# Performance work log

Measured on AMD Instinct MI355X. Metric: run time of the kernel, lower is better.

## Reference

```python
import jax, jax.numpy as jnp
import numpy as np

NUM_CODES = 1024
CODE_DIM = 256
COMMIT_W = 0.25
EPS = 1e-5
ENT_LO, ENT_HI = 0.5, 0.9
ENT_W = 0.1
VAR_FLOOR = 0.05
VAR_W = 1e-3
DECORR_W = 1e-3


def setup_inputs() -> dict:
    key = jax.random.key(0)
    k1, k2, k3 = jax.random.split(key, 3)
    inputs = jax.random.normal(k1, (16, 2048, CODE_DIM), dtype=jnp.float32)
    weight = jax.random.normal(k2, (NUM_CODES, CODE_DIM), dtype=jnp.float32) * 0.1
    usage_counts = jax.random.uniform(k3, (NUM_CODES,), dtype=jnp.float32)
    return {"inputs": inputs, "weight": weight, "usage_counts": usage_counts}


def reference(inputs, weight, usage_counts):
    K, D = weight.shape
    flat = inputs.reshape(-1, D)  # [N, D]
    # squared euclidean distances [N, K]
    dist = (flat ** 2).sum(axis=1, keepdims=True) - 2.0 * flat @ weight.T + (weight ** 2).sum(axis=1)
    idx = jnp.argmin(dist, axis=1)  # [N]
    quant = weight[idx].reshape(inputs.shape)

    commitment_loss = COMMIT_W * jnp.mean((jax.lax.stop_gradient(quant) - inputs) ** 2)
    # straight-through estimator
    quant_ste = inputs + jax.lax.stop_gradient(quant - inputs)

    # usage entropy regularizer
    probs = usage_counts + EPS
    probs = probs / jnp.maximum(probs.sum(), EPS * K)
    usage_entropy = -jnp.sum(probs * jnp.log(probs + EPS)) / np.log(float(K)).astype(np.float32)
    gap = jnp.where(usage_entropy < ENT_LO, ENT_LO - usage_entropy,
                    jnp.where(usage_entropy > ENT_HI, usage_entropy - ENT_HI, 0.0))
    entropy_loss = ENT_W * gap ** 2

    # variance floor penalty on codebook
    variance = jnp.var(weight, axis=0)
    variance_loss = VAR_W * jnp.mean(jax.nn.relu(VAR_FLOOR - variance))

    # decorrelation penalty
    wc = weight - weight.mean(axis=0, keepdims=True)
    cov = wc.T @ wc / float(K)  # [D, D]
    off_diag = cov - jnp.diag(jnp.diag(cov))
    decorrelation_loss = DECORR_W * jnp.mean(off_diag ** 2)

    total_loss = commitment_loss + entropy_loss + variance_loss + decorrelation_loss
    indices = idx.reshape(inputs.shape[:-1])
    return (quant_ste, indices, total_loss, commitment_loss, entropy_loss,
            variance_loss, decorrelation_loss, usage_entropy)
```

## Files before the change

### kernel.cpp

```cpp
#include <hip/hip_runtime.h>
#include <math.h>

#define DIMS   256
#define KCODES 1024
#define NTOT   32768
#define TAU    4.0e-4f

typedef __bf16 bf16x8 __attribute__((ext_vector_type(8)));
typedef float  f32x4  __attribute__((ext_vector_type(4)));

#define WS_COMMIT   0
#define WS_FLAGCNT  1
#define WS_DECORR   2
#define WS_COLSUM   16
#define WS_COLSQ    272
#define WS_WSQ      1024
#define WS_XSQ      2048
#define WS_FLAGS    34816
#define WS_CAND1    67584
#define WS_CAND2    329728
#define WS_CANDI    591872
#define WS_WP       854016

#define OUT_Q    0
#define OUT_IDX  8388608
#define OUT_SCAL 8421376


__global__ __launch_bounds__(256) void prep_kernel(const float* __restrict__ X,
                                                   const float* __restrict__ W,
                                                   __bf16* __restrict__ Xp,
                                                   __bf16* __restrict__ Wp2,
                                                   float* ws) {
  int b = blockIdx.x;
  int tid = threadIdx.x;
  if (b < 1056) {
    __shared__ float sqred[256];
    bool isW = b >= 1024;
    const float* src = isW ? W : X;
    __bf16* dst = isW ? Wp2 : Xp;
    int sqoff = isW ? WS_WSQ : WS_XSQ;
    int bb = isW ? b - 1024 : b;
    int kt = tid >> 5, mtl = (tid >> 4) & 1, lc = tid & 15;
    int row = bb * 32 + mtl * 16 + lc;
    int bt = row >> 7, c = row & 127;
    int wv = c >> 6, t = (c >> 4) & 3;
    size_t hibase = ((((size_t)(bt * 8 + kt) * 2 + wv) * 4 + t) * 2) * 512;
    const float* s = src + (size_t)row * DIMS + kt * 32;
    float sq = 0.f;
    #pragma unroll
    for (int kq = 0; kq < 4; kq++) {
      float4 u = *(const float4*)(s + kq * 8);
      float4 v = *(const float4*)(s + kq * 8 + 4);
      float f[8] = {u.x, u.y, u.z, u.w, v.x, v.y, v.z, v.w};
      bf16x8 hi, lo;
      #pragma unroll
      for (int e = 0; e < 8; e++) {
        __bf16 h = (__bf16)f[e];
        hi[e] = h;
        lo[e] = (__bf16)(f[e] - (float)h);
        sq = fmaf(f[e], f[e], sq);
      }
      size_t off = (size_t)(kq * 16 + lc) * 8;
      *(bf16x8*)&dst[hibase + off] = hi;
      *(bf16x8*)&dst[hibase + 512 + off] = lo;
    }
    sqred[tid] = sq;
    __syncthreads();
    if (tid < 32) {
      float s8 = 0.f;
      #pragma unroll
      for (int k = 0; k < 8; k++) s8 += sqred[k * 32 + tid];
      ws[sqoff + bb * 32 + tid] = s8;
    }
  } else {
    __shared__ float wi_s[KCODES];
    __shared__ float red2[256];
    __shared__ float miB;
    __shared__ float red[4];
    int i0 = b - 1056;
    #pragma unroll
    for (int q = 0; q < 4; q++) {
      int row = q * 256 + tid;
      wi_s[row] = W[(size_t)row * DIMS + i0];
    }
    __syncthreads();
    float pm = 0.f;
    #pragma unroll
    for (int q = 0; q < 4; q++) pm += wi_s[tid * 4 + q];
    red2[tid] = pm;
    __syncthreads();
    if (tid == 0) {
      float s = 0.f;
      for (int k = 0; k < 256; k++) s += red2[k];
      miB = s * (1.0f / 1024.0f);
    }
    int j = tid;
    float a0 = 0.f, sj = 0.f, sqj = 0.f;
    for (int k = 0; k < KCODES; k += 4) {
      #pragma unroll
      for (int u = 0; u < 4; u++) {
        float wj = W[(size_t)(k + u) * DIMS + j];
        a0 = fmaf(wi_s[k + u], wj, a0);
        sj += wj;
        sqj = fmaf(wj, wj, sqj);
      }
    }
    if (j == i0) {
      ws[WS_COLSUM + i0] = sj;
      ws[WS_COLSQ + i0] = sqj;
    }
    __syncthreads();
    const float inv = 1.0f / 1024.0f;
    float mj = sj * inv;
    float v = 0.f;
    float c0 = a0 * inv - miB * mj;
    if (i0 != j) v = c0 * c0;
    #pragma unroll
    for (int m = 32; m >= 1; m >>= 1) v += __shfl_xor(v, m);
    if ((j & 63) == 0) red[j >> 6] = v;
    __syncthreads();
    if (j == 0) atomicAdd(&ws[WS_DECORR], (red[0] + red[1]) + (red[2] + red[3]));
  }
}

__global__ __launch_bounds__(256, 2) void pass1_kernel(const __bf16* __restrict__ Xp,
                                                       const __bf16* __restrict__ Wp2,
                                                       float* ws) {
  __shared__ float wsqs[128];
  __shared__ float d1L[256];
  __shared__ float d2L[256];
  __shared__ int   i1L[256];

  int tid = threadIdx.x;
  int lane = tid & 63, wave = tid >> 6;
  int wm = wave >> 1, wn = wave & 1;
  int quad = lane >> 4, col = lane & 15;
  int l = blockIdx.x;
  int x = l & 7;
  int j = l >> 3;
  int bm = x * 32 + (j & 15) + (j >> 7) * 16;
  int bn = (j >> 4) & 7;
  int rowBase = bm * 128, cb = bn * 128;

  if (tid < 128) wsqs[tid] = ws[WS_WSQ + cb + tid];

  f32x4 acc[4][4];
  #pragma unroll
  for (int i = 0; i < 4; i++)
    #pragma unroll
    for (int jj = 0; jj < 4; jj++) acc[i][jj] = (f32x4){0.f, 0.f, 0.f, 0.f};

  const bf16x8* ab = (const bf16x8*)(Xp + (size_t)bm * 65536 + wm * 4096) + lane;
  const bf16x8* bb = (const bf16x8*)(Wp2 + (size_t)bn * 65536 + wn * 4096) + lane;

  bf16x8 Af[2][8], Bf[2][8];
  #pragma unroll
  for (int f = 0; f < 4; f++) {
    Af[0][f * 2] = ab[f * 128];
    Af[0][f * 2 + 1] = ab[f * 128 + 64];
    Bf[0][f * 2] = bb[f * 128];
    Bf[0][f * 2 + 1] = bb[f * 128 + 64];
  }
  #pragma unroll
  for (int kt = 0; kt < 8; kt++) {
    const int cur = kt & 1, nxt = cur ^ 1;
    if (kt < 7) {
      const bf16x8* an = ab + (kt + 1) * 1024;
      const bf16x8* bv = bb + (kt + 1) * 1024;
      #pragma unroll
      for (int f = 0; f < 4; f++) {
        Af[nxt][f * 2] = an[f * 128];
        Af[nxt][f * 2 + 1] = an[f * 128 + 64];
        Bf[nxt][f * 2] = bv[f * 128];
        Bf[nxt][f * 2 + 1] = bv[f * 128 + 64];
      }
    }
    #pragma unroll
    for (int nt = 0; nt < 4; nt++) {
      #pragma unroll
      for (int mt = 0; mt < 4; mt++) {
        acc[mt][nt] = __builtin_amdgcn_mfma_f32_16x16x32_bf16(Af[cur][mt * 2], Bf[cur][nt * 2], acc[mt][nt], 0, 0, 0);
        acc[mt][nt] = __builtin_amdgcn_mfma_f32_16x16x32_bf16(Af[cur][mt * 2], Bf[cur][nt * 2 + 1], acc[mt][nt], 0, 0, 0);
        acc[mt][nt] = __builtin_amdgcn_mfma_f32_16x16x32_bf16(Af[cur][mt * 2 + 1], Bf[cur][nt * 2], acc[mt][nt], 0, 0, 0);
      }
    }
  }
  __syncthreads();

  #pragma unroll
  for (int mt = 0; mt < 4; mt++) {
    #pragma unroll
    for (int r = 0; r < 4; r++) {
      float d1 = 3.0e38f, d2 = 3.0e38f;
      int i1 = 0;
      #pragma unroll
      for (int nt = 0; nt < 4; nt++) {
        int lc = wn * 64 + nt * 16 + col;
        float d = wsqs[lc] - 2.0f * acc[mt][nt][r];
        int g = cb + lc;
        if (d < d1) { d2 = d1; d1 = d; i1 = g; }
        else if (d < d2) d2 = d;
      }
      #pragma unroll
      for (int m = 1; m < 16; m <<= 1) {
        float od1 = __shfl_xor(d1, m);
        int oi1 = __shfl_xor(i1, m);
        float od2 = __shfl_xor(d2, m);
        if (od1 < d1 || (od1 == d1 && oi1 < i1)) {
          d2 = fminf(d1, fminf(d2, od2));
          d1 = od1; i1 = oi1;
        } else {
          d2 = fminf(od1, fminf(d2, od2));
        }
      }
      if (col == 0) {
        int lr = wm * 64 + mt * 16 + quad * 4 + r;
        d1L[lr * 2 + wn] = d1;
        d2L[lr * 2 + wn] = d2;
        i1L[lr * 2 + wn] = i1;
      }
    }
  }
  __syncthreads();
  if (tid < 128) {
    float a1 = d1L[tid * 2], a2 = d2L[tid * 2];
    int ai = i1L[tid * 2];
    float b1 = d1L[tid * 2 + 1], b2 = d2L[tid * 2 + 1];
    int bi = i1L[tid * 2 + 1];
    float m1, m2; int mi;
    if (b1 < a1 || (b1 == a1 && bi < ai)) { m1 = b1; mi = bi; m2 = fminf(a1, b2); }
    else { m1 = a1; mi = ai; m2 = fminf(b1, a2); }
    int o = bn * NTOT + rowBase + tid;
    ws[WS_CAND1 + o] = m1;
    ws[WS_CAND2 + o] = m2;
    ((int*)ws)[WS_CANDI + o] = mi;
  }
}

__global__ __launch_bounds__(256) void pass2_kernel(const float* __restrict__ W,
                                                    float* __restrict__ outQ,
                                                    float* __restrict__ outIdx, float* ws) {
  __shared__ float p1L[4][64];
  __shared__ float p2L[4][64];
  __shared__ int   piL[4][64];
  __shared__ int   idx_s[64];
  int tid = threadIdx.x;
  int r0 = blockIdx.x * 64;
  int grp = tid >> 6, rl = tid & 63;
  int row = r0 + rl;
  const float* c1 = ws + WS_CAND1;
  const float* c2 = ws + WS_CAND2;
  const int* ci = (const int*)ws + WS_CANDI;
  {
    int oa = (2 * grp) * NTOT + row;
    int ob = (2 * grp + 1) * NTOT + row;
    float a1 = c1[oa], a2 = c2[oa];
    int ai = ci[oa];
    float b1 = c1[ob], b2 = c2[ob];
    int bi = ci[ob];
    float m1, m2; int mi;
    if (b1 < a1 || (b1 == a1 && bi < ai)) { m1 = b1; mi = bi; m2 = fminf(a1, b2); }
    else { m1 = a1; mi = ai; m2 = fminf(a2, b1); }
    p1L[grp][rl] = m1;
    p2L[grp][rl] = m2;
    piL[grp][rl] = mi;
  }
  __syncthreads();
  if (tid < 64) {
    float m1 = p1L[0][tid], m2 = p2L[0][tid];
    int mi = piL[0][tid];
    #pragma unroll
    for (int w = 1; w < 4; w++) {
      float b1 = p1L[w][tid], b2 = p2L[w][tid];
      int bi = piL[w][tid];
      if (b1 < m1 || (b1 == m1 && bi < mi)) { m2 = fminf(m1, b2); m1 = b1; mi = bi; }
      else { m2 = fminf(m2, b1); }
    }
    int rw = r0 + tid;
    outIdx[rw] = (float)mi;
    idx_s[tid] = mi;
    int* wsI = (int*)ws;
    if (m2 - m1 < TAU) {
      int p = atomicAdd(&wsI[WS_FLAGCNT], 1);
      wsI[WS_FLAGS + p] = rw;
    }
    float partial = ws[WS_XSQ + rw] + m1;
    #pragma unroll
    for (int m = 32; m >= 1; m >>= 1) partial += __shfl_xor(partial, m);
    if (tid == 0) atomicAdd(&ws[WS_COMMIT], partial);
  }
  __syncthreads();
  int wave = tid >> 6, lane = tid & 63;
  #pragma unroll 4
  for (int i = 0; i < 16; i++) {
    int rr = wave * 16 + i;
    int ix = idx_s[rr];
    float4 v = ((const float4*)(W + (size_t)ix * DIMS))[lane];
    ((float4*)(outQ + (size_t)(r0 + rr) * DIMS))[lane] = v;
  }
}

__global__ __launch_bounds__(256) void refine_kernel(const float* __restrict__ X,
                                                     const float* __restrict__ W,
                                                     float* __restrict__ outQ,
                                                     float* __restrict__ outIdx, float* ws,
                                                     const float* __restrict__ U,
                                                     float* __restrict__ out) {
  __shared__ float xs[DIMS];
  __shared__ double dm[256];
  __shared__ int im[256];
  __shared__ int chosen;
  int tid = threadIdx.x;
  if (blockIdx.x == 512) {
    __shared__ float red[256];
    float s = 0.f;
    for (int e = tid; e < KCODES; e += 256) s += U[e] + 1e-5f;
    red[tid] = s;
    __syncthreads();
    for (int st = 128; st >= 1; st >>= 1) {
      if (tid < st) red[tid] += red[tid + st];
      __syncthreads();
    }
    float S = red[0];
    __syncthreads();
    float denom = fmaxf(S, 1e-5f * 1024.0f);
    float h = 0.f;
    for (int e = tid; e < KCODES; e += 256) {
      float p = (U[e] + 1e-5f) / denom;
      h += p * logf(p + 1e-5f);
    }
    red[tid] = h;
    __syncthreads();
    for (int st = 128; st >= 1; st >>= 1) {
      if (tid < st) red[tid] += red[tid + st];
      __syncthreads();
    }
    float H = -red[0] / 6.93147180559945f;
    __syncthreads();
    float m = ws[WS_COLSUM + tid] * (1.0f / 1024.0f);
    float var = ws[WS_COLSQ + tid] * (1.0f / 1024.0f) - m * m;
    float r = 0.05f - var;
    red[tid] = r > 0.f ? r : 0.f;
    __syncthreads();
    for (int st = 128; st >= 1; st >>= 1) {
      if (tid < st) red[tid] += red[tid + st];
      __syncthreads();
    }
    if (tid == 0) {
      float varloss = 1e-3f * (red[0] / 256.0f);
      float gap = H < 0.5f ? (0.5f - H) : (H > 0.9f ? (H - 0.9f) : 0.0f);
      float entloss = 0.1f * gap * gap;
      float commit = 0.25f * ws[WS_COMMIT] / 8388608.0f;
      float dec = 1e-3f * ws[WS_DECORR] / 65536.0f;
      float* sc = out + OUT_SCAL;
      sc[0] = commit + entloss + varloss + dec;
      sc[1] = commit;
      sc[2] = entloss;
      sc[3] = varloss;
      sc[4] = dec;
      sc[5] = H;
    }
    return;
  }
  const int* wsI = (const int*)ws;
  int cnt = wsI[WS_FLAGCNT];
  const int* list = wsI + WS_FLAGS;
  for (int f = blockIdx.x; f < cnt; f += 512) {
    int row = list[f];
    __syncthreads();
    if (tid < 64) ((float4*)xs)[tid] = ((const float4*)(X + (size_t)row * DIMS))[tid];
    __syncthreads();
    double bd = 1.0e300;
    int bi = 0;
    for (int jj = 0; jj < 4; jj++) {
      int c = tid + 256 * jj;
      double a0 = 0.0, a1 = 0.0, a2 = 0.0, a3 = 0.0;
      const float* wr = W + (size_t)c * DIMS;
      #pragma unroll 4
      for (int d4 = 0; d4 < 64; d4++) {
        float4 w = ((const float4*)wr)[d4];
        float4 x = ((const float4*)xs)[d4];
        double e0 = (double)x.x - (double)w.x;
        double e1 = (double)x.y - (double)w.y;
        double e2 = (double)x.z - (double)w.z;
        double e3 = (double)x.w - (double)w.w;
        a0 += e0 * e0; a1 += e1 * e1; a2 += e2 * e2; a3 += e3 * e3;
      }
      double s = (a0 + a1) + (a2 + a3);
      if (s < bd) { bd = s; bi = c; }
    }
    dm[tid] = bd; im[tid] = bi;
    __syncthreads();
    for (int st = 128; st >= 1; st >>= 1) {
      if (tid < st) {
        if (dm[tid + st] < dm[tid] || (dm[tid + st] == dm[tid] && im[tid + st] < im[tid])) {
          dm[tid] = dm[tid + st]; im[tid] = im[tid + st];
        }
      }
      __syncthreads();
    }
    if (tid == 0) { chosen = im[0]; outIdx[row] = (float)im[0]; }
    __syncthreads();
    int ix = chosen;
    if (tid < 64)
      ((float4*)(outQ + (size_t)row * DIMS))[tid] = ((const float4*)(W + (size_t)ix * DIMS))[tid];
  }
}

extern "C" void kernel_launch(void* const* d_in, const int* in_sizes, int n_in, void* d_out,
                              int out_size, void* d_ws, size_t ws_size, hipStream_t stream) {
  const float* X = (const float*)d_in[0];
  const float* W = (const float*)d_in[1];
  const float* U = (const float*)d_in[2];
  float* out = (float*)d_out;
  float* ws = (float*)d_ws;
  __bf16* Xp = (__bf16*)(out + OUT_Q);
  __bf16* Wp2 = (__bf16*)(ws + WS_WP);

  hipMemsetAsync(d_ws, 0, 12, stream);
  prep_kernel<<<1312, 256, 0, stream>>>(X, W, Xp, Wp2, ws);
  pass1_kernel<<<2048, 256, 0, stream>>>(Xp, Wp2, ws);
  pass2_kernel<<<512, 256, 0, stream>>>(W, out + OUT_Q, out + OUT_IDX, ws);
  refine_kernel<<<513, 256, 0, stream>>>(X, W, out + OUT_Q, out + OUT_IDX, ws, U, out);
}
```

Baseline: 229.2 us.

## Stage pass1 GEMM tiles through LDS via global_load_lds instead of register prefetch

The distance GEMM in pass1 used to load A and B fragments straight from global memory into registers, double-buffered. It now copies each k-tile of both operands into a 32KB shared buffer with direct global-to-LDS loads, then reads the fragments from LDS. Each tile is loaded once per block and shared across the waves, which should cut redundant global traffic and register pressure. Occupancy hint is raised from 2 to 3 blocks. The price is single-buffered staging with two barriers per k-step and no overlap of loads with MFMA work.

```diff
diff --git a/kernel.cpp b/kernel.cpp
--- a/kernel.cpp
+++ b/kernel.cpp
@@ -124,9 +124,16 @@
   }
 }
 
-__global__ __launch_bounds__(256, 2) void pass1_kernel(const __bf16* __restrict__ Xp,
+__device__ __forceinline__ void stage16(const __bf16* g, __bf16* l) {
+  __builtin_amdgcn_global_load_lds(
+      (const __attribute__((address_space(1))) void*)g,
+      (__attribute__((address_space(3))) void*)l, 16, 0, 0);
+}
+
+__global__ __launch_bounds__(256, 3) void pass1_kernel(const __bf16* __restrict__ Xp,
                                                        const __bf16* __restrict__ Wp2,
                                                        float* ws) {
+  __shared__ __align__(16) __bf16 buf[16384];
   __shared__ float wsqs[128];
   __shared__ float d1L[256];
   __shared__ float d2L[256];
@@ -151,38 +158,36 @@
     #pragma unroll
     for (int jj = 0; jj < 4; jj++) acc[i][jj] = (f32x4){0.f, 0.f, 0.f, 0.f};
 
-  const bf16x8* ab = (const bf16x8*)(Xp + (size_t)bm * 65536 + wm * 4096) + lane;
-  const bf16x8* bb = (const bf16x8*)(Wp2 + (size_t)bn * 65536 + wn * 4096) + lane;
-
-  bf16x8 Af[2][8], Bf[2][8];
-  #pragma unroll
-  for (int f = 0; f < 4; f++) {
-    Af[0][f * 2] = ab[f * 128];
-    Af[0][f * 2 + 1] = ab[f * 128 + 64];
-    Bf[0][f * 2] = bb[f * 128];
-    Bf[0][f * 2 + 1] = bb[f * 128 + 64];
-  }
+  const __bf16* aSrc = Xp + (size_t)bm * 65536;
+  const __bf16* bSrc = Wp2 + (size_t)bn * 65536;
+
   #pragma unroll
   for (int kt = 0; kt < 8; kt++) {
-    const int cur = kt & 1, nxt = cur ^ 1;
-    if (kt < 7) {
-      const bf16x8* an = ab + (kt + 1) * 1024;
-      const bf16x8* bv = bb + (kt + 1) * 1024;
-      #pragma unroll
-      for (int f = 0; f < 4; f++) {
-        Af[nxt][f * 2] = an[f * 128];
-        Af[nxt][f * 2 + 1] = an[f * 128 + 64];
-        Bf[nxt][f * 2] = bv[f * 128];
-        Bf[nxt][f * 2 + 1] = bv[f * 128 + 64];
-      }
-    }
+    __syncthreads();
+    #pragma unroll
+    for (int q = 0; q < 4; q++) {
+      stage16(aSrc + kt * 8192 + q * 2048 + tid * 8, buf + q * 2048 + tid * 8);
+      stage16(bSrc + kt * 8192 + q * 2048 + tid * 8, buf + 8192 + q * 2048 + tid * 8);
+    }
+    __syncthreads();
+
+    const __bf16* bA = buf + wm * 4096 + lane * 8;
+    const __bf16* bB = buf + 8192 + wn * 4096 + lane * 8;
+    bf16x8 Bf[4][2];
     #pragma unroll
     for (int nt = 0; nt < 4; nt++) {
-      #pragma unroll
-      for (int mt = 0; mt < 4; mt++) {
-        acc[mt][nt] = __builtin_amdgcn_mfma_f32_16x16x32_bf16(Af[cur][mt * 2], Bf[cur][nt * 2], acc[mt][nt], 0, 0, 0);
-        acc[mt][nt] = __builtin_amdgcn_mfma_f32_16x16x32_bf16(Af[cur][mt * 2], Bf[cur][nt * 2 + 1], acc[mt][nt], 0, 0, 0);
-        acc[mt][nt] = __builtin_amdgcn_mfma_f32_16x16x32_bf16(Af[cur][mt * 2 + 1], Bf[cur][nt * 2], acc[mt][nt], 0, 0, 0);
+      Bf[nt][0] = *(const bf16x8*)(bB + nt * 1024);
+      Bf[nt][1] = *(const bf16x8*)(bB + nt * 1024 + 512);
+    }
+    #pragma unroll
+    for (int mt = 0; mt < 4; mt++) {
+      bf16x8 A0 = *(const bf16x8*)(bA + mt * 1024);
+      bf16x8 A1 = *(const bf16x8*)(bA + mt * 1024 + 512);
+      #pragma unroll
+      for (int nt = 0; nt < 4; nt++) {
+        acc[mt][nt] = __builtin_amdgcn_mfma_f32_16x16x32_bf16(A0, Bf[nt][0], acc[mt][nt], 0, 0, 0);
+        acc[mt][nt] = __builtin_amdgcn_mfma_f32_16x16x32_bf16(A0, Bf[nt][1], acc[mt][nt], 0, 0, 0);
+        acc[mt][nt] = __builtin_amdgcn_mfma_f32_16x16x32_bf16(A1, Bf[nt][0], acc[mt][nt], 0, 0, 0);
       }
     }
   }
```

Result: slower. 236.3 us (+3.1%).
